# Kernel optimization log

Hardware: AMD Instinct MI355X
Metric: run time of the kernel (lower is better)

The kernel has to match this reference:

```python
import jax, jax.numpy as jnp
import numpy as np

NUM_ROUTING = 3

def squash(v, axis=-1):
    s = jnp.sum(jnp.square(v), axis=axis, keepdims=True)
    scale = s / (1.0 + s) / jnp.sqrt(s)
    return scale * v

def setup_inputs() -> dict:
    key = jax.random.key(0)
    k1, k2 = jax.random.split(key)
    B, IN_CAPS, IN_DIM = 32, 1152, 64
    NUM_CAPS, OUT_DIM = 32, 64
    x = jax.random.normal(k1, (B, IN_CAPS, IN_DIM), dtype=jnp.float32)
    W = jax.random.normal(k2, (IN_CAPS, NUM_CAPS, IN_DIM, OUT_DIM), dtype=jnp.float32) * 0.05
    bias = jnp.zeros((1, IN_CAPS, NUM_CAPS, 1), dtype=jnp.float32)
    return {"x": x, "W": W, "bias": bias}

def reference(x, W, bias):
    # x: [B, i, p], W: [i, c, p, q] -> inputs_hat: [B, i, c, q]
    # (equivalent to the tf.scan of per-sample batch_dot, vectorized)
    inputs_hat = jnp.einsum('bip,icpq->bicq', x, W)
    b = bias  # [1, i, c, 1] -> broadcasts to [B, i, c, 1] after first update
    outputs = None
    for r in range(NUM_ROUTING):
        c = jax.nn.softmax(b, axis=2)                       # softmax over output capsules
        outputs = squash(jnp.sum(c * inputs_hat, axis=1, keepdims=True))  # [B, 1, c, q]
        if r != NUM_ROUTING - 1:
            b = b + jnp.sum(inputs_hat * outputs, axis=-1, keepdims=True)
    num_caps, out_dim = W.shape[1], W.shape[3]
    return outputs.reshape(-1, num_caps, out_dim)
```

## Files before the change

### kernel.cpp

```cpp
#include <hip/hip_runtime.h>
#include <hip/hip_fp16.h>

#define BB 32
#define IN_CAPS 1152
#define IN_DIM 64
#define NUM_CAPS 32
#define OUT_DIM 64
#define NCOL 2048
#define ICHUNK 32
#define NCHUNK 36

#define HAT_ELEMS  ((size_t)BB * IN_CAPS * NCOL)
#define OFF_PART   (HAT_ELEMS * 2)
#define PART_ELEMS ((size_t)NCHUNK * BB * NCOL)
#define OFF_LOGIT  (OFF_PART + PART_ELEMS * 4)
#define LOGIT_ELEMS ((size_t)BB * IN_CAPS * NUM_CAPS)
#define OFF_OUT1   (OFF_LOGIT + LOGIT_ELEMS * 4)
#define OFF_OUT2   (OFF_OUT1 + (size_t)BB * NCOL * 4)

__global__ __launch_bounds__(256, 2)
void gemm_hat(const float* __restrict__ x, const float* __restrict__ W,
              __half* __restrict__ hat)
{
    const int i = blockIdx.y;
    const int colbase = blockIdx.x * 1024 + threadIdx.x * 4;
    const int c  = colbase >> 6;
    const int q0 = colbase & 63;

    __shared__ float xt[IN_DIM][BB];
    {
        const int t  = threadIdx.x;
        const int b  = t >> 3;
        const int pg = (t & 7) * 8;
        const float* xp = x + ((size_t)b * IN_CAPS + i) * IN_DIM + pg;
        float4 v0 = *(const float4*)xp;
        float4 v1 = *(const float4*)(xp + 4);
        xt[pg + 0][b] = v0.x; xt[pg + 1][b] = v0.y;
        xt[pg + 2][b] = v0.z; xt[pg + 3][b] = v0.w;
        xt[pg + 4][b] = v1.x; xt[pg + 5][b] = v1.y;
        xt[pg + 6][b] = v1.z; xt[pg + 7][b] = v1.w;
    }
    __syncthreads();

    float4 acc[BB];
    #pragma unroll
    for (int b = 0; b < BB; ++b) acc[b] = make_float4(0.f, 0.f, 0.f, 0.f);

    const float* wp = W + ((size_t)i * NUM_CAPS + c) * IN_DIM * OUT_DIM + q0;
    #pragma unroll 4
    for (int p = 0; p < IN_DIM; ++p) {
        const float4 w4 = *(const float4*)wp; wp += OUT_DIM;
        #pragma unroll
        for (int bg = 0; bg < 8; ++bg) {
            const float4 xv = *(const float4*)(&xt[p][bg * 4]);
            acc[bg*4+0].x += xv.x * w4.x; acc[bg*4+0].y += xv.x * w4.y;
            acc[bg*4+0].z += xv.x * w4.z; acc[bg*4+0].w += xv.x * w4.w;
            acc[bg*4+1].x += xv.y * w4.x; acc[bg*4+1].y += xv.y * w4.y;
            acc[bg*4+1].z += xv.y * w4.z; acc[bg*4+1].w += xv.y * w4.w;
            acc[bg*4+2].x += xv.z * w4.x; acc[bg*4+2].y += xv.z * w4.y;
            acc[bg*4+2].z += xv.z * w4.z; acc[bg*4+2].w += xv.z * w4.w;
            acc[bg*4+3].x += xv.w * w4.x; acc[bg*4+3].y += xv.w * w4.y;
            acc[bg*4+3].z += xv.w * w4.z; acc[bg*4+3].w += xv.w * w4.w;
        }
    }

    #pragma unroll
    for (int b = 0; b < BB; ++b) {
        const float4 a = acc[b];
        __half2 h01 = __floats2half2_rn(a.x, a.y);
        __half2 h23 = __floats2half2_rn(a.z, a.w);
        uint2 pk;
        pk.x = *reinterpret_cast<unsigned int*>(&h01);
        pk.y = *reinterpret_cast<unsigned int*>(&h23);
        *reinterpret_cast<uint2*>(hat + ((size_t)b * IN_CAPS + i) * NCOL + colbase) = pk;
    }
}

template<int ROUND>
__global__ __launch_bounds__(256, 2)
void route_pass(const __half* __restrict__ hat,
                const float* __restrict__ out_prev,
                const float* __restrict__ logits_in,
                float* __restrict__ logits_out,
                float* __restrict__ partials)
{
    const int chunk = blockIdx.x;
    const int b     = blockIdx.y;
    const int wave  = threadIdx.x >> 6;
    const int lane  = threadIdx.x & 63;
    const int g     = lane >> 3;
    const int q0    = (lane & 7) * 8;

    float outv[4][8];
    if (ROUND >= 2) {
        #pragma unroll
        for (int k = 0; k < 4; ++k) {
            const int c = 8 * k + g;
            const float* op = out_prev + ((size_t)b * NUM_CAPS + c) * OUT_DIM + q0;
            float4 o0 = *(const float4*)op;
            float4 o1 = *(const float4*)(op + 4);
            outv[k][0] = o0.x; outv[k][1] = o0.y; outv[k][2] = o0.z; outv[k][3] = o0.w;
            outv[k][4] = o1.x; outv[k][5] = o1.y; outv[k][6] = o1.z; outv[k][7] = o1.w;
        }
    }

    float acc[4][8];
    #pragma unroll
    for (int k = 0; k < 4; ++k)
        #pragma unroll
        for (int j = 0; j < 8; ++j) acc[k][j] = 0.f;

    for (int t = 0; t < 8; ++t) {
        const int i = chunk * ICHUNK + wave * 8 + t;
        const __half* hp = hat + ((size_t)b * IN_CAPS + i) * NCOL;

        float hf[4][8];
        #pragma unroll
        for (int k = 0; k < 4; ++k) {
            float4 raw = *(const float4*)(hp + k * 512 + lane * 8);
            union { float4 f; __half2 h[4]; } u; u.f = raw;
            #pragma unroll
            for (int j2 = 0; j2 < 4; ++j2) {
                float2 fv = __half22float2(u.h[j2]);
                hf[k][2 * j2]     = fv.x;
                hf[k][2 * j2 + 1] = fv.y;
            }
        }

        float lg[4];
        if (ROUND == 1) {
            #pragma unroll
            for (int k = 0; k < 4; ++k)
                lg[k] = logits_in[i * NUM_CAPS + 8 * k + g];
        } else {
            float d[4];
            #pragma unroll
            for (int k = 0; k < 4; ++k) {
                float s = 0.f;
                #pragma unroll
                for (int j = 0; j < 8; ++j) s += hf[k][j] * outv[k][j];
                s += __shfl_xor(s, 1);
                s += __shfl_xor(s, 2);
                s += __shfl_xor(s, 4);
                d[k] = s;
            }
            #pragma unroll
            for (int k = 0; k < 4; ++k) {
                if (ROUND == 2)
                    lg[k] = logits_in[i * NUM_CAPS + 8 * k + g] + d[k];
                else
                    lg[k] = logits_in[((size_t)b * IN_CAPS + i) * NUM_CAPS + 8 * k + g] + d[k];
            }
            if (ROUND == 2 && (lane & 7) == 0) {
                #pragma unroll
                for (int k = 0; k < 4; ++k)
                    logits_out[((size_t)b * IN_CAPS + i) * NUM_CAPS + 8 * k + g] = lg[k];
            }
        }

        float mx = fmaxf(fmaxf(lg[0], lg[1]), fmaxf(lg[2], lg[3]));
        mx = fmaxf(mx, __shfl_xor(mx, 8));
        mx = fmaxf(mx, __shfl_xor(mx, 16));
        mx = fmaxf(mx, __shfl_xor(mx, 32));
        float ex[4];
        float se = 0.f;
        #pragma unroll
        for (int k = 0; k < 4; ++k) { ex[k] = __expf(lg[k] - mx); se += ex[k]; }
        se += __shfl_xor(se, 8);
        se += __shfl_xor(se, 16);
        se += __shfl_xor(se, 32);
        const float inv = 1.0f / se;

        #pragma unroll
        for (int k = 0; k < 4; ++k) {
            const float cc = ex[k] * inv;
            #pragma unroll
            for (int j = 0; j < 8; ++j) acc[k][j] += cc * hf[k][j];
        }
    }

    __shared__ float red[4][NCOL];
    #pragma unroll
    for (int k = 0; k < 4; ++k)
        #pragma unroll
        for (int j = 0; j < 8; ++j)
            red[wave][(8 * k + g) * 64 + q0 + j] = acc[k][j];
    __syncthreads();

    for (int e = threadIdx.x; e < NCOL; e += 256) {
        float s = red[0][e] + red[1][e] + red[2][e] + red[3][e];
        partials[((size_t)chunk * BB + b) * NCOL + e] = s;
    }
}

__global__ __launch_bounds__(256)
void reduce_squash(const float* __restrict__ partials, float* __restrict__ out)
{
    const int gw   = blockIdx.x * 4 + (threadIdx.x >> 6);
    const int lane = threadIdx.x & 63;
    const int b = gw >> 5;
    const int c = gw & 31;

    float s = 0.f;
    #pragma unroll 4
    for (int k = 0; k < NCHUNK; ++k)
        s += partials[((size_t)k * BB + b) * NCOL + c * OUT_DIM + lane];

    float sq = s * s;
    #pragma unroll
    for (int m = 1; m < 64; m <<= 1) sq += __shfl_xor(sq, m);

    const float scale = sq / (1.f + sq) * rsqrtf(sq);
    out[((size_t)b * NUM_CAPS + c) * OUT_DIM + lane] = s * scale;
}

extern "C" void kernel_launch(void* const* d_in, const int* in_sizes, int n_in,
                              void* d_out, int out_size, void* d_ws, size_t ws_size,
                              hipStream_t stream)
{
    const float* x    = (const float*)d_in[0];
    const float* W    = (const float*)d_in[1];
    const float* bias = (const float*)d_in[2];
    float* out = (float*)d_out;

    char* ws = (char*)d_ws;
    __half* hat     = (__half*)ws;
    float* partials = (float*)(ws + OFF_PART);
    float* logits   = (float*)(ws + OFF_LOGIT);
    float* out1     = (float*)(ws + OFF_OUT1);
    float* out2     = (float*)(ws + OFF_OUT2);

    gemm_hat<<<dim3(2, IN_CAPS), 256, 0, stream>>>(x, W, hat);

    route_pass<1><<<dim3(NCHUNK, BB), 256, 0, stream>>>(hat, nullptr, bias, nullptr, partials);
    reduce_squash<<<256, 256, 0, stream>>>(partials, out1);

    route_pass<2><<<dim3(NCHUNK, BB), 256, 0, stream>>>(hat, out1, bias, logits, partials);
    reduce_squash<<<256, 256, 0, stream>>>(partials, out2);

    route_pass<3><<<dim3(NCHUNK, BB), 256, 0, stream>>>(hat, out2, logits, nullptr, partials);
    reduce_squash<<<256, 256, 0, stream>>>(partials, out);
}
```

Measured before the change: 889.9 us.

## Fuse routing rounds into one cooperative kernel and drop stored logits

Merges the three routing passes and their reductions into a single cooperative kernel that uses grid-wide syncs in place of six separate launches. It stops storing per-batch logits by using the identity b3 = bias + hat·(out1+out2), so round 3 reads two small output arrays instead of a large logits buffer. It also halves the number of chunks, so each block covers 64 input capsules and the partials buffer is smaller. The cost is grid-sync overhead and a residency requirement of 576 blocks. If the cooperative launch fails, the code falls back to separate launches.

```diff
diff --git a/kernel.cpp b/kernel.cpp
--- a/kernel.cpp
+++ b/kernel.cpp
@@ -1,5 +1,8 @@
 #include <hip/hip_runtime.h>
 #include <hip/hip_fp16.h>
+#include <hip/hip_cooperative_groups.h>
+
+namespace cg = cooperative_groups;
 
 #define BB 32
 #define IN_CAPS 1152
@@ -7,15 +10,13 @@
 #define NUM_CAPS 32
 #define OUT_DIM 64
 #define NCOL 2048
-#define ICHUNK 32
-#define NCHUNK 36
-
-#define HAT_ELEMS  ((size_t)BB * IN_CAPS * NCOL)
-#define OFF_PART   (HAT_ELEMS * 2)
-#define PART_ELEMS ((size_t)NCHUNK * BB * NCOL)
-#define OFF_LOGIT  (OFF_PART + PART_ELEMS * 4)
-#define LOGIT_ELEMS ((size_t)BB * IN_CAPS * NUM_CAPS)
-#define OFF_OUT1   (OFF_LOGIT + LOGIT_ELEMS * 4)
+#define NCHUNK 18
+#define ICHUNK 64
+
+#define HAT_BYTES  ((size_t)BB * IN_CAPS * NCOL * 2)
+#define OFF_PART   (HAT_BYTES)
+#define PART_BYTES ((size_t)NCHUNK * BB * NCOL * 4)
+#define OFF_OUT1   (OFF_PART + PART_BYTES)
 #define OFF_OUT2   (OFF_OUT1 + (size_t)BB * NCOL * 4)
 
 __global__ __launch_bounds__(256, 2)
@@ -76,31 +77,32 @@
     }
 }
 
-template<int ROUND>
-__global__ __launch_bounds__(256, 2)
-void route_pass(const __half* __restrict__ hat,
-                const float* __restrict__ out_prev,
-                const float* __restrict__ logits_in,
-                float* __restrict__ logits_out,
-                float* __restrict__ partials)
-{
-    const int chunk = blockIdx.x;
-    const int b     = blockIdx.y;
-    const int wave  = threadIdx.x >> 6;
-    const int lane  = threadIdx.x & 63;
-    const int g     = lane >> 3;
-    const int q0    = (lane & 7) * 8;
+__device__ __forceinline__
+void round_body(const __half* __restrict__ hat, const float* __restrict__ bias,
+                const float* __restrict__ oA, const float* __restrict__ oB,
+                float* __restrict__ partials,
+                int cp, int b, int wave, int lane, float (*red)[NCOL])
+{
+    const int g  = lane >> 3;
+    const int q0 = (lane & 7) * 8;
 
     float outv[4][8];
-    if (ROUND >= 2) {
+    if (oA) {
         #pragma unroll
         for (int k = 0; k < 4; ++k) {
             const int c = 8 * k + g;
-            const float* op = out_prev + ((size_t)b * NUM_CAPS + c) * OUT_DIM + q0;
+            const float* op = oA + ((size_t)b * NUM_CAPS + c) * OUT_DIM + q0;
             float4 o0 = *(const float4*)op;
             float4 o1 = *(const float4*)(op + 4);
             outv[k][0] = o0.x; outv[k][1] = o0.y; outv[k][2] = o0.z; outv[k][3] = o0.w;
             outv[k][4] = o1.x; outv[k][5] = o1.y; outv[k][6] = o1.z; outv[k][7] = o1.w;
+            if (oB) {
+                const float* op2 = oB + ((size_t)b * NUM_CAPS + c) * OUT_DIM + q0;
+                float4 p0 = *(const float4*)op2;
+                float4 p1 = *(const float4*)(op2 + 4);
+                outv[k][0] += p0.x; outv[k][1] += p0.y; outv[k][2] += p0.z; outv[k][3] += p0.w;
+                outv[k][4] += p1.x; outv[k][5] += p1.y; outv[k][6] += p1.z; outv[k][7] += p1.w;
+            }
         }
     }
 
@@ -110,8 +112,8 @@
         #pragma unroll
         for (int j = 0; j < 8; ++j) acc[k][j] = 0.f;
 
-    for (int t = 0; t < 8; ++t) {
-        const int i = chunk * ICHUNK + wave * 8 + t;
+    for (int t = 0; t < 16; ++t) {
+        const int i = cp * ICHUNK + wave * 16 + t;
         const __half* hp = hat + ((size_t)b * IN_CAPS + i) * NCOL;
 
         float hf[4][8];
@@ -128,12 +130,10 @@
         }
 
         float lg[4];
-        if (ROUND == 1) {
-            #pragma unroll
-            for (int k = 0; k < 4; ++k)
-                lg[k] = logits_in[i * NUM_CAPS + 8 * k + g];
-        } else {
-            float d[4];
+        #pragma unroll
+        for (int k = 0; k < 4; ++k)
+            lg[k] = bias[i * NUM_CAPS + 8 * k + g];
+        if (oA) {
             #pragma unroll
             for (int k = 0; k < 4; ++k) {
                 float s = 0.f;
@@ -142,19 +142,7 @@
                 s += __shfl_xor(s, 1);
                 s += __shfl_xor(s, 2);
                 s += __shfl_xor(s, 4);
-                d[k] = s;
-            }
-            #pragma unroll
-            for (int k = 0; k < 4; ++k) {
-                if (ROUND == 2)
-                    lg[k] = logits_in[i * NUM_CAPS + 8 * k + g] + d[k];
-                else
-                    lg[k] = logits_in[((size_t)b * IN_CAPS + i) * NUM_CAPS + 8 * k + g] + d[k];
-            }
-            if (ROUND == 2 && (lane & 7) == 0) {
-                #pragma unroll
-                for (int k = 0; k < 4; ++k)
-                    logits_out[((size_t)b * IN_CAPS + i) * NUM_CAPS + 8 * k + g] = lg[k];
+                lg[k] += s;
             }
         }
 
@@ -179,7 +167,6 @@
         }
     }
 
-    __shared__ float red[4][NCOL];
     #pragma unroll
     for (int k = 0; k < 4; ++k)
         #pragma unroll
@@ -187,31 +174,77 @@
             red[wave][(8 * k + g) * 64 + q0 + j] = acc[k][j];
     __syncthreads();
 
-    for (int e = threadIdx.x; e < NCOL; e += 256) {
+    const int tid = wave * 64 + lane;
+    for (int e = tid; e < NCOL; e += 256) {
         float s = red[0][e] + red[1][e] + red[2][e] + red[3][e];
-        partials[((size_t)chunk * BB + b) * NCOL + e] = s;
-    }
-}
-
-__global__ __launch_bounds__(256)
-void reduce_squash(const float* __restrict__ partials, float* __restrict__ out)
-{
-    const int gw   = blockIdx.x * 4 + (threadIdx.x >> 6);
-    const int lane = threadIdx.x & 63;
-    const int b = gw >> 5;
-    const int c = gw & 31;
+        partials[((size_t)cp * BB + b) * NCOL + e] = s;
+    }
+}
+
+__device__ __forceinline__
+void reduce_body(const float* __restrict__ partials, float* __restrict__ dst,
+                 int w, int lane)
+{
+    if (w >= BB * NUM_CAPS) return;
+    const int b = w >> 5;
+    const int c = w & 31;
 
     float s = 0.f;
-    #pragma unroll 4
+    #pragma unroll 6
     for (int k = 0; k < NCHUNK; ++k)
         s += partials[((size_t)k * BB + b) * NCOL + c * OUT_DIM + lane];
 
     float sq = s * s;
     #pragma unroll
     for (int m = 1; m < 64; m <<= 1) sq += __shfl_xor(sq, m);
+    sq = fmaxf(sq, 1e-20f);
 
     const float scale = sq / (1.f + sq) * rsqrtf(sq);
-    out[((size_t)b * NUM_CAPS + c) * OUT_DIM + lane] = s * scale;
+    dst[((size_t)b * NUM_CAPS + c) * OUT_DIM + lane] = s * scale;
+}
+
+__global__ __launch_bounds__(256, 3)
+void routing_all(const __half* __restrict__ hat, const float* __restrict__ bias,
+                 float* __restrict__ partials, float* __restrict__ out1,
+                 float* __restrict__ out2, float* __restrict__ outF)
+{
+    cg::grid_group grid = cg::this_grid();
+    __shared__ float red[4][NCOL];
+
+    const int unit = blockIdx.x;
+    const int cp   = unit % NCHUNK;
+    const int b    = unit / NCHUNK;
+    const int wave = threadIdx.x >> 6;
+    const int lane = threadIdx.x & 63;
+    const int w    = unit * 4 + wave;
+
+    const float* oa[3] = { nullptr, out1, out1 };
+    const float* ob[3] = { nullptr, nullptr, out2 };
+    float*       ds[3] = { out1, out2, outF };
+
+    for (int r = 0; r < 3; ++r) {
+        round_body(hat, bias, oa[r], ob[r], partials, cp, b, wave, lane, red);
+        grid.sync();
+        reduce_body(partials, ds[r], w, lane);
+        grid.sync();
+    }
+}
+
+__global__ __launch_bounds__(256, 3)
+void route_k(const __half* __restrict__ hat, const float* __restrict__ bias,
+             const float* __restrict__ oA, const float* __restrict__ oB,
+             float* __restrict__ partials)
+{
+    __shared__ float red[4][NCOL];
+    round_body(hat, bias, oA, oB, partials,
+               blockIdx.x % NCHUNK, blockIdx.x / NCHUNK,
+               threadIdx.x >> 6, threadIdx.x & 63, red);
+}
+
+__global__ __launch_bounds__(256)
+void reduce_k(const float* __restrict__ partials, float* __restrict__ dst)
+{
+    reduce_body(partials, dst, blockIdx.x * 4 + (threadIdx.x >> 6), threadIdx.x & 63);
 }
 
 extern "C" void kernel_launch(void* const* d_in, const int* in_sizes, int n_in,
@@ -226,18 +259,21 @@
     char* ws = (char*)d_ws;
     __half* hat     = (__half*)ws;
     float* partials = (float*)(ws + OFF_PART);
-    float* logits   = (float*)(ws + OFF_LOGIT);
     float* out1     = (float*)(ws + OFF_OUT1);
     float* out2     = (float*)(ws + OFF_OUT2);
 
     gemm_hat<<<dim3(2, IN_CAPS), 256, 0, stream>>>(x, W, hat);
 
-    route_pass<1><<<dim3(NCHUNK, BB), 256, 0, stream>>>(hat, nullptr, bias, nullptr, partials);
-    reduce_squash<<<256, 256, 0, stream>>>(partials, out1);
-
-    route_pass<2><<<dim3(NCHUNK, BB), 256, 0, stream>>>(hat, out1, bias, logits, partials);
-    reduce_squash<<<256, 256, 0, stream>>>(partials, out2);
-
-    route_pass<3><<<dim3(NCHUNK, BB), 256, 0, stream>>>(hat, out2, logits, nullptr, partials);
-    reduce_squash<<<256, 256, 0, stream>>>(partials, out);
-}
+    void* args[6] = { (void*)&hat, (void*)&bias, (void*)&partials,
+                      (void*)&out1, (void*)&out2, (void*)&out };
+    hipError_t e = hipLaunchCooperativeKernel((const void*)routing_all,
+                                              dim3(576), dim3(256), args, 0, stream);
+    if (e != hipSuccess) {
+        route_k<<<576, 256, 0, stream>>>(hat, bias, nullptr, nullptr, partials);
+        reduce_k<<<256, 256, 0, stream>>>(partials, out1);
+        route_k<<<576, 256, 0, stream>>>(hat, bias, out1, nullptr, partials);
+        reduce_k<<<256, 256, 0, stream>>>(partials, out2);
+        route_k<<<576, 256, 0, stream>>>(hat, bias, out1, out2, partials);
+        reduce_k<<<256, 256, 0, stream>>>(partials, out);
+    }
+}
```

Result: slower. 1.272 ms (+42.9%).
